# Kernel tuning notes

Hardware: AMD Instinct MI355X
Metric: run time of the kernel (lower is better)

## Reference

```python
import jax, jax.numpy as jnp
import numpy as np

N_QUBITS = 10
T_STEPS = 10
NDATA = 1024
DIM = 2 ** N_QUBITS
PI = float(np.pi)


def setup_inputs() -> dict:
    key = jax.random.key(0)
    k1, k2, k3, k4, k5 = jax.random.split(key, 5)
    # random complex amplitudes (normalized to unit states inside reference)
    inputs_re = jax.random.normal(k1, (NDATA, DIM), dtype=jnp.float32)
    inputs_im = jax.random.normal(k2, (NDATA, DIM), dtype=jnp.float32)
    # diffusion noise schedule diff_hs (t,) in (0,1]
    diff_hs = jax.random.uniform(k5, (T_STEPS,), dtype=jnp.float32, minval=0.1, maxval=1.0)
    # var_1 = diff_hs.repeat(3n) in torch == tile -> index k scaled by diff_hs[k % t]
    var_1 = jnp.tile(diff_hs, 3 * N_QUBITS)                                  # (3*n*t,)
    phis = (jax.random.uniform(k3, (NDATA, 3 * N_QUBITS * T_STEPS), dtype=jnp.float32)
            * (PI / 4.0) - (PI / 8.0)) * var_1[None, :]
    gs = (jax.random.uniform(k4, (NDATA, T_STEPS), dtype=jnp.float32) * 0.2 + 0.4) * diff_hs[None, :]
    return {"inputs_re": inputs_re, "inputs_im": inputs_im, "phis": phis, "gs": gs}


def _apply_1q(psi, M, i):
    """Apply per-sample 2x2 gate M (B,2,2) on qubit i (qubit 0 = MSB) to psi (B, 2**n)."""
    left = 2 ** i
    right = 2 ** (N_QUBITS - 1 - i)
    s = psi.reshape(NDATA, left, 2, right)
    s = jnp.einsum('bxy,bayc->baxc', M, s)
    return s.reshape(NDATA, DIM)


def _scramble(inputs_re, inputs_im, phis, gs):
    n, t = N_QUBITS, T_STEPS
    psi = (inputs_re + 1j * inputs_im).astype(jnp.complex64)
    psi = psi / jnp.linalg.norm(psi, axis=1, keepdims=True)  # unit input states

    # precompute sum_{i<j} z_i z_j per basis state for the diagonal RZZ product
    idx = jnp.arange(DIM)
    bits = (idx[:, None] >> jnp.arange(n - 1, -1, -1)[None, :]) & 1  # (DIM, n), qubit0=MSB
    z = 1.0 - 2.0 * bits.astype(jnp.float32)
    zsum = z.sum(axis=1)
    pairsum = 0.5 * (zsum ** 2 - n)                                   # (DIM,)
    inv = 1.0 / (2.0 * np.sqrt(float(n)))

    for tt in range(t):
        base = 3 * n * tt
        for i in range(n):
            a = phis[:, base + i]            # first RZ angle
            th = phis[:, base + n + i]       # RY angle
            b = phis[:, base + 2 * n + i]    # second RZ angle
            c = jnp.cos(0.5 * th).astype(jnp.complex64)
            s = jnp.sin(0.5 * th).astype(jnp.complex64)
            ea_m = jnp.exp(-0.5j * a); ea_p = jnp.exp(0.5j * a)
            eb_m = jnp.exp(-0.5j * b); eb_p = jnp.exp(0.5j * b)
            # M = RZ(b) @ RY(th) @ RZ(a), per sample (B,2,2)
            M = jnp.stack([
                jnp.stack([eb_m * c * ea_m, -eb_m * s * ea_p], axis=-1),
                jnp.stack([eb_p * s * ea_m,  eb_p * c * ea_p], axis=-1),
            ], axis=-2)
            psi = _apply_1q(psi, M, i)
        # all RZZ(i,j, theta) gates are diagonal with shared theta -> single fused phase
        theta = (gs[:, tt] * inv).astype(jnp.complex64)
        psi = psi * jnp.exp(-0.5j * theta[:, None] * pairsum[None, :])
    return psi


def reference(inputs_re, inputs_im, phis, gs):
    psi = _scramble(inputs_re, inputs_im, phis, gs)
    return jnp.stack([psi.real, psi.imag])  # (2, Ndata, 2**n) float32
```

## Files before the change

### kernel.cpp

```cpp
#include <hip/hip_runtime.h>

#define NQ 10
#define TS 10
#define DIM 1024
#define ND 1024

typedef _Float16 h4 __attribute__((ext_vector_type(4)));
typedef __fp16  p2 __attribute__((ext_vector_type(2)));
typedef float f4 __attribute__((ext_vector_type(4)));

__device__ __forceinline__ f4 mfma16(h4 a, h4 b, f4 c) {
    return __builtin_amdgcn_mfma_f32_16x16x16f16(a, b, c, 0, 0, 0);
}
__device__ __forceinline__ h4 cvt_h4(f4 x) {
    p2 lo = __builtin_amdgcn_cvt_pkrtz(x[0], x[1]);
    p2 hi = __builtin_amdgcn_cvt_pkrtz(x[2], x[3]);
    h4 r; r[0] = lo[0]; r[1] = lo[1]; r[2] = hi[0]; r[3] = hi[1];
    return r;
}
__device__ __forceinline__ float hsel(int ob, int ib, float cq, float sq) {
    return (ob == ib) ? cq : (ob ? sq : -sq);
}

__global__ __launch_bounds__(64, 1) void qsim_kernel(
    const float* __restrict__ re_in, const float* __restrict__ im_in,
    const float* __restrict__ phis, const float* __restrict__ gs,
    float* __restrict__ out)
{
    const int sample = blockIdx.x;
    const int lane = threadIdx.x;
    const int quad = lane >> 4;
    const int cc = lane & 15;
    const int c3 = (cc >> 3) & 1, c2 = (cc >> 2) & 1, c1 = (cc >> 1) & 1, c0 = cc & 1;
    const int q1 = quad >> 1, q0 = quad & 1;

    const float* pr_in = re_in + sample * DIM;
    const float* pi_in = im_in + sample * DIM;
    const float* ph = phis + sample * (3 * NQ * TS);
    const float* gsp = gs + sample * TS;

    f4 Sr[4], Si[4];
    const int lbase = 256 * quad + cc;
#pragma unroll
    for (int n = 0; n < 4; ++n)
#pragma unroll
        for (int s = 0; s < 4; ++s) {
            Sr[n][s] = pr_in[lbase + 64 * s + 16 * n];
            Si[n][s] = pi_in[lbase + 64 * s + 16 * n];
        }

    const float inv = 0.15811388300841897f;
    float gk[TS];
#pragma unroll
    for (int t = 0; t < TS; ++t) gk[t] = -0.5f * (gsp[t] * inv);

    float nrm = 0.f;
#pragma unroll
    for (int n = 0; n < 4; ++n)
#pragma unroll
        for (int s = 0; s < 4; ++s) nrm += Sr[n][s] * Sr[n][s] + Si[n][s] * Si[n][s];
#pragma unroll
    for (int off = 32; off >= 1; off >>= 1) nrm += __shfl_xor(nrm, off, 64);
    const float scl = rsqrtf(nrm);
#pragma unroll
    for (int n = 0; n < 4; ++n) { Sr[n] *= scl; Si[n] *= scl; }

    float psv[4][4];
    const int pbase = __popc(quad) + __popc(cc);
#pragma unroll
    for (int n = 0; n < 4; ++n)
#pragma unroll
        for (int s = 0; s < 4; ++s) {
            const int p = pbase + __popc(n) + __popc(s);
            const int z = NQ - 2 * p;
            psv[n][s] = 0.5f * (float)(z * z - NQ);
        }
    const float fq1 = (float)q1, fq0 = (float)q0;
    const float fc3 = (float)c3, fc2 = (float)c2, fc1 = (float)c1, fc0 = (float)c0;

    float DCP[4][4], DSP[4][4];
    h4 gb; h4 hb[4][4];
    float bcur[NQ];

    auto make_trig = [&](const float* v, float kcur, float dcp[4][4], float dsp[4][4]) {
        float sv = 0.f;
#pragma unroll
        for (int i = 0; i < NQ; ++i) sv += v[i];
        float base = fmaf(-0.5f, sv, 0.f);
        base = fmaf(fq1, v[0], base); base = fmaf(fq0, v[1], base);
        base = fmaf(fc3, v[6], base); base = fmaf(fc2, v[7], base);
        base = fmaf(fc1, v[8], base); base = fmaf(fc0, v[9], base);
        const float addS[4] = {0.f, v[3], v[2], v[2] + v[3]};
        const float addN[4] = {0.f, v[5], v[4], v[4] + v[5]};
#pragma unroll
        for (int n = 0; n < 4; ++n)
#pragma unroll
            for (int s = 0; s < 4; ++s) {
                const float phi = fmaf(kcur, psv[n][s], base + addN[n] + addS[s]);
                float sp, cp;
                __sincosf(phi, &sp, &cp);
                dcp[n][s] = cp;
                dsp[n][s] = sp;
            }
    };
    auto make_tiles = [&](const float* th_src, h4& gbo, h4 hbo[4][4]) {
        float C[NQ], S[NQ];
#pragma unroll
        for (int g = 0; g < NQ; ++g) {
            float sg, cg;
            __sincosf(0.5f * th_src[g], &sg, &cg);
            S[g] = sg; C[g] = cg;
        }
        {
            const float f01 = hsel(c3, q1, C[0], S[0]) * hsel(c2, q0, C[1], S[1]);
            float e[4];
#pragma unroll
            for (int s = 0; s < 4; ++s)
                e[s] = f01 * hsel(c1, s >> 1, C[2], S[2]) * hsel(c0, s & 1, C[3], S[3]);
            p2 lo = __builtin_amdgcn_cvt_pkrtz(e[0], e[1]);
            p2 hi = __builtin_amdgcn_cvt_pkrtz(e[2], e[3]);
            gbo[0] = lo[0]; gbo[1] = lo[1]; gbo[2] = hi[0]; gbo[3] = hi[1];
        }
        const float F67 = hsel(c3, q1, C[6], S[6]) * hsel(c2, q0, C[7], S[7]);
        float F89[4];
#pragma unroll
        for (int s = 0; s < 4; ++s)
            F89[s] = F67 * hsel(c1, s >> 1, C[8], S[8]) * hsel(c0, s & 1, C[9], S[9]);
#pragma unroll
        for (int n = 0; n < 4; ++n)
#pragma unroll
            for (int j = 0; j < 4; ++j) {
                const float F45 = hsel(n >> 1, j >> 1, C[4], S[4])
                                * hsel(n & 1,  j & 1,  C[5], S[5]);
                p2 lo = __builtin_amdgcn_cvt_pkrtz(F45 * F89[0], F45 * F89[1]);
                p2 hi = __builtin_amdgcn_cvt_pkrtz(F45 * F89[2], F45 * F89[3]);
                hbo[n][j][0] = lo[0]; hbo[n][j][1] = lo[1];
                hbo[n][j][2] = hi[0]; hbo[n][j][3] = hi[1];
            }
    };

    {
        float phs0[30];
#pragma unroll
        for (int j = 0; j < 30; ++j) phs0[j] = ph[j];
        make_trig(&phs0[0], 0.f, DCP, DSP);
        make_tiles(&phs0[10], gb, hb);
#pragma unroll
        for (int i = 0; i < NQ; ++i) bcur[i] = phs0[20 + i];
    }
    float pipe[2][30];
#pragma unroll
    for (int j = 0; j < 30; ++j) pipe[0][j] = ph[30 + j];

    const f4 zf4 = {0.f, 0.f, 0.f, 0.f};

#pragma unroll
    for (int tt = 0; tt < TS; ++tt) {
#pragma unroll
        for (int n = 0; n < 4; ++n)
#pragma unroll
            for (int s = 0; s < 4; ++s) {
                const float cp = DCP[n][s], sp = DSP[n][s];
                const float xr = Sr[n][s], xi = Si[n][s];
                Sr[n][s] = cp * xr - sp * xi;
                Si[n][s] = sp * xr + cp * xi;
            }

        if (tt + 2 < TS) {
#pragma unroll
            for (int j = 0; j < 30; ++j) pipe[(tt + 1) & 1][j] = ph[30 * (tt + 2) + j];
        }

        h4 ar[4], ai[4];
#pragma unroll
        for (int n = 0; n < 4; ++n) { ar[n] = cvt_h4(Sr[n]); ai[n] = cvt_h4(Si[n]); }
        f4 Tr[4], Ti[4];
#pragma unroll
        for (int n = 0; n < 4; ++n) {
            Tr[n] = mfma16(ar[n], gb, zf4);
            Ti[n] = mfma16(ai[n], gb, zf4);
        }
        h4 tr[4], ti[4];
#pragma unroll
        for (int n = 0; n < 4; ++n) { tr[n] = cvt_h4(Tr[n]); ti[n] = cvt_h4(Ti[n]); }
#pragma unroll
        for (int n = 0; n < 4; ++n) {
            f4 accr = zf4, acci = zf4;
#pragma unroll
            for (int j = 0; j < 4; ++j) {
                accr = mfma16(tr[j], hb[n][j], accr);
                acci = mfma16(ti[j], hb[n][j], acci);
            }
            Sr[n] = accr;
            Si[n] = acci;
        }

        if (tt + 1 < TS) {
            const float* pN = pipe[tt & 1];
            float vN[NQ];
#pragma unroll
            for (int i = 0; i < NQ; ++i) vN[i] = pN[i] + bcur[i];
            make_trig(vN, gk[tt], DCP, DSP);
            make_tiles(&pN[10], gb, hb);
#pragma unroll
            for (int i = 0; i < NQ; ++i) bcur[i] = pN[20 + i];
        } else {
            make_trig(bcur, gk[TS - 1], DCP, DSP);
        }
    }

#pragma unroll
    for (int n = 0; n < 4; ++n)
#pragma unroll
        for (int s = 0; s < 4; ++s) {
            const float cp = DCP[n][s], sp = DSP[n][s];
            const float xr = Sr[n][s], xi = Si[n][s];
            Sr[n][s] = cp * xr - sp * xi;
            Si[n][s] = sp * xr + cp * xi;
        }

    float* outr = out + sample * DIM;
    float* outi = out + ND * DIM + sample * DIM;
#pragma unroll
    for (int n = 0; n < 4; ++n)
#pragma unroll
        for (int s = 0; s < 4; ++s) {
            outr[lbase + 64 * s + 16 * n] = Sr[n][s];
            outi[lbase + 64 * s + 16 * n] = Si[n][s];
        }
}

extern "C" void kernel_launch(void* const* d_in, const int* in_sizes, int n_in,
                              void* d_out, int out_size, void* d_ws, size_t ws_size,
                              hipStream_t stream) {
    const float* re_in = (const float*)d_in[0];
    const float* im_in = (const float*)d_in[1];
    const float* phis  = (const float*)d_in[2];
    const float* gs    = (const float*)d_in[3];
    float* out = (float*)d_out;
    qsim_kernel<<<ND, 64, 0, stream>>>(re_in, im_in, phis, gs, out);
}
```

Before: 77.83 us.

## Double-buffer gate tiles and interleave next-step trig with MFMA chains

Gate tile registers become double-buffered so the next step's trig and tile construction can be placed between the first and second MFMA stages. This hides transcendental and ALU latency behind matrix work. The second-stage accumulation is split into two independent chains that are summed afterward, which shortens the MFMA dependency chain. The sign-select helper is replaced by sign-bit XOR and shared product tables, which cuts per-step ALU work at the cost of more register pressure from the duplicated tiles.

Result: no change. 77.47 us (-0.5%).

```diff
diff --git a/kernel.cpp b/kernel.cpp
--- a/kernel.cpp
+++ b/kernel.cpp
@@ -18,8 +18,8 @@
     h4 r; r[0] = lo[0]; r[1] = lo[1]; r[2] = hi[0]; r[3] = hi[1];
     return r;
 }
-__device__ __forceinline__ float hsel(int ob, int ib, float cq, float sq) {
-    return (ob == ib) ? cq : (ob ? sq : -sq);
+__device__ __forceinline__ float xsgn(float v, unsigned m) {
+    return __uint_as_float(__float_as_uint(v) ^ m);
 }
 
 __global__ __launch_bounds__(64, 1) void qsim_kernel(
@@ -34,6 +34,13 @@
     const int c3 = (cc >> 3) & 1, c2 = (cc >> 2) & 1, c1 = (cc >> 1) & 1, c0 = cc & 1;
     const int q1 = quad >> 1, q0 = quad & 1;
 
+    const bool e31 = (c3 == q1);
+    const bool e20 = (c2 == q0);
+    const bool bc1 = (c1 != 0);
+    const bool bc0 = (c0 != 0);
+    const unsigned sg3 = c3 ? 0u : 0x80000000u;
+    const unsigned sg2 = c2 ? 0u : 0x80000000u;
+
     const float* pr_in = re_in + sample * DIM;
     const float* pi_in = im_in + sample * DIM;
     const float* ph = phis + sample * (3 * NQ * TS);
@@ -78,15 +85,16 @@
     const float fq1 = (float)q1, fq0 = (float)q0;
     const float fc3 = (float)c3, fc2 = (float)c2, fc1 = (float)c1, fc0 = (float)c0;
 
-    float DCP[4][4], DSP[4][4];
-    h4 gb; h4 hb[4][4];
+    f4 DCPv[4], DSPv[4];
+    h4 gbb[2];
+    h4 hbb[2][4][4];
     float bcur[NQ];
 
-    auto make_trig = [&](const float* v, float kcur, float dcp[4][4], float dsp[4][4]) {
+    auto make_trig = [&](const float* v, float kcur) {
         float sv = 0.f;
 #pragma unroll
         for (int i = 0; i < NQ; ++i) sv += v[i];
-        float base = fmaf(-0.5f, sv, 0.f);
+        float base = -0.5f * sv;
         base = fmaf(fq1, v[0], base); base = fmaf(fq0, v[1], base);
         base = fmaf(fc3, v[6], base); base = fmaf(fc2, v[7], base);
         base = fmaf(fc1, v[8], base); base = fmaf(fc0, v[9], base);
@@ -99,41 +107,55 @@
                 const float phi = fmaf(kcur, psv[n][s], base + addN[n] + addS[s]);
                 float sp, cp;
                 __sincosf(phi, &sp, &cp);
-                dcp[n][s] = cp;
-                dsp[n][s] = sp;
+                DCPv[n][s] = cp;
+                DSPv[n][s] = sp;
             }
     };
-    auto make_tiles = [&](const float* th_src, h4& gbo, h4 hbo[4][4]) {
+
+    auto make_tiles = [&](const float* th, h4& gbo, h4 (&hbo)[4][4]) {
         float C[NQ], S[NQ];
 #pragma unroll
         for (int g = 0; g < NQ; ++g) {
             float sg, cg;
-            __sincosf(0.5f * th_src[g], &sg, &cg);
+            __sincosf(0.5f * th[g], &sg, &cg);
             S[g] = sg; C[g] = cg;
         }
         {
-            const float f01 = hsel(c3, q1, C[0], S[0]) * hsel(c2, q0, C[1], S[1]);
-            float e[4];
-#pragma unroll
-            for (int s = 0; s < 4; ++s)
-                e[s] = f01 * hsel(c1, s >> 1, C[2], S[2]) * hsel(c0, s & 1, C[3], S[3]);
-            p2 lo = __builtin_amdgcn_cvt_pkrtz(e[0], e[1]);
-            p2 hi = __builtin_amdgcn_cvt_pkrtz(e[2], e[3]);
+            const float g0 = e31 ? C[0] : xsgn(S[0], sg3);
+            const float g1 = e20 ? C[1] : xsgn(S[1], sg2);
+            const float f01 = g0 * g1;
+            const float A0 = bc1 ? S[2] : C[2];
+            const float A1 = bc1 ? C[2] : -S[2];
+            const float B0 = bc0 ? S[3] : C[3];
+            const float B1 = bc0 ? C[3] : -S[3];
+            p2 lo = __builtin_amdgcn_cvt_pkrtz(f01 * A0 * B0, f01 * A0 * B1);
+            p2 hi = __builtin_amdgcn_cvt_pkrtz(f01 * A1 * B0, f01 * A1 * B1);
             gbo[0] = lo[0]; gbo[1] = lo[1]; gbo[2] = hi[0]; gbo[3] = hi[1];
         }
-        const float F67 = hsel(c3, q1, C[6], S[6]) * hsel(c2, q0, C[7], S[7]);
-        float F89[4];
-#pragma unroll
-        for (int s = 0; s < 4; ++s)
-            F89[s] = F67 * hsel(c1, s >> 1, C[8], S[8]) * hsel(c0, s & 1, C[9], S[9]);
+        const float F67 = (e31 ? C[6] : xsgn(S[6], sg3)) * (e20 ? C[7] : xsgn(S[7], sg2));
+        const float A0p = bc1 ? S[8] : C[8];
+        const float A1p = bc1 ? C[8] : -S[8];
+        const float B0p = bc0 ? S[9] : C[9];
+        const float B1p = bc0 ? C[9] : -S[9];
+        float W[4];
+        W[0] = F67 * A0p * B0p; W[1] = F67 * A0p * B1p;
+        W[2] = F67 * A1p * B0p; W[3] = F67 * A1p * B1p;
+        const float P4[4] = {C[4] * C[5], C[4] * S[5], S[4] * C[5], S[4] * S[5]};
+        float TP[4][4];
+#pragma unroll
+        for (int k = 0; k < 4; ++k)
+#pragma unroll
+            for (int s = 0; s < 4; ++s) TP[k][s] = P4[k] * W[s];
 #pragma unroll
         for (int n = 0; n < 4; ++n)
 #pragma unroll
             for (int j = 0; j < 4; ++j) {
-                const float F45 = hsel(n >> 1, j >> 1, C[4], S[4])
-                                * hsel(n & 1,  j & 1,  C[5], S[5]);
-                p2 lo = __builtin_amdgcn_cvt_pkrtz(F45 * F89[0], F45 * F89[1]);
-                p2 hi = __builtin_amdgcn_cvt_pkrtz(F45 * F89[2], F45 * F89[3]);
+                const int n1 = n >> 1, n0 = n & 1, j1 = j >> 1, j0 = j & 1;
+                const int d1 = n1 ^ j1, d0 = n0 ^ j0;
+                const int idx = d1 * 2 + d0;
+                const float sg = (((d1 && !n1) ? -1.f : 1.f) * ((d0 && !n0) ? -1.f : 1.f));
+                p2 lo = __builtin_amdgcn_cvt_pkrtz(sg * TP[idx][0], sg * TP[idx][1]);
+                p2 hi = __builtin_amdgcn_cvt_pkrtz(sg * TP[idx][2], sg * TP[idx][3]);
                 hbo[n][j][0] = lo[0]; hbo[n][j][1] = lo[1];
                 hbo[n][j][2] = hi[0]; hbo[n][j][3] = hi[1];
             }
@@ -143,8 +165,8 @@
         float phs0[30];
 #pragma unroll
         for (int j = 0; j < 30; ++j) phs0[j] = ph[j];
-        make_trig(&phs0[0], 0.f, DCP, DSP);
-        make_tiles(&phs0[10], gb, hb);
+        make_trig(&phs0[0], 0.f);
+        make_tiles(&phs0[10], gbb[0], hbb[0]);
 #pragma unroll
         for (int i = 0; i < NQ; ++i) bcur[i] = phs0[20 + i];
     }
@@ -157,14 +179,11 @@
 #pragma unroll
     for (int tt = 0; tt < TS; ++tt) {
 #pragma unroll
-        for (int n = 0; n < 4; ++n)
-#pragma unroll
-            for (int s = 0; s < 4; ++s) {
-                const float cp = DCP[n][s], sp = DSP[n][s];
-                const float xr = Sr[n][s], xi = Si[n][s];
-                Sr[n][s] = cp * xr - sp * xi;
-                Si[n][s] = sp * xr + cp * xi;
-            }
+        for (int n = 0; n < 4; ++n) {
+            const f4 xr = Sr[n], xi = Si[n];
+            Sr[n] = DCPv[n] * xr - DSPv[n] * xi;
+            Si[n] = DSPv[n] * xr + DCPv[n] * xi;
+        }
 
         if (tt + 2 < TS) {
 #pragma unroll
@@ -177,22 +196,8 @@
         f4 Tr[4], Ti[4];
 #pragma unroll
         for (int n = 0; n < 4; ++n) {
-            Tr[n] = mfma16(ar[n], gb, zf4);
-            Ti[n] = mfma16(ai[n], gb, zf4);
-        }
-        h4 tr[4], ti[4];
-#pragma unroll
-        for (int n = 0; n < 4; ++n) { tr[n] = cvt_h4(Tr[n]); ti[n] = cvt_h4(Ti[n]); }
-#pragma unroll
-        for (int n = 0; n < 4; ++n) {
-            f4 accr = zf4, acci = zf4;
-#pragma unroll
-            for (int j = 0; j < 4; ++j) {
-                accr = mfma16(tr[j], hb[n][j], accr);
-                acci = mfma16(ti[j], hb[n][j], acci);
-            }
-            Sr[n] = accr;
-            Si[n] = acci;
+            Tr[n] = mfma16(ar[n], gbb[tt & 1], zf4);
+            Ti[n] = mfma16(ai[n], gbb[tt & 1], zf4);
         }
 
         if (tt + 1 < TS) {
@@ -200,24 +205,38 @@
             float vN[NQ];
 #pragma unroll
             for (int i = 0; i < NQ; ++i) vN[i] = pN[i] + bcur[i];
-            make_trig(vN, gk[tt], DCP, DSP);
-            make_tiles(&pN[10], gb, hb);
+            make_trig(vN, gk[tt]);
+            make_tiles(&pN[10], gbb[(tt + 1) & 1], hbb[(tt + 1) & 1]);
 #pragma unroll
             for (int i = 0; i < NQ; ++i) bcur[i] = pN[20 + i];
         } else {
-            make_trig(bcur, gk[TS - 1], DCP, DSP);
+            make_trig(bcur, gk[TS - 1]);
+        }
+
+        h4 tr[4], ti[4];
+#pragma unroll
+        for (int n = 0; n < 4; ++n) { tr[n] = cvt_h4(Tr[n]); ti[n] = cvt_h4(Ti[n]); }
+#pragma unroll
+        for (int n = 0; n < 4; ++n) {
+            f4 r0 = mfma16(tr[0], hbb[tt & 1][n][0], zf4);
+            r0 = mfma16(tr[1], hbb[tt & 1][n][1], r0);
+            f4 r1 = mfma16(tr[2], hbb[tt & 1][n][2], zf4);
+            r1 = mfma16(tr[3], hbb[tt & 1][n][3], r1);
+            f4 i0 = mfma16(ti[0], hbb[tt & 1][n][0], zf4);
+            i0 = mfma16(ti[1], hbb[tt & 1][n][1], i0);
+            f4 i1 = mfma16(ti[2], hbb[tt & 1][n][2], zf4);
+            i1 = mfma16(ti[3], hbb[tt & 1][n][3], i1);
+            Sr[n] = r0 + r1;
+            Si[n] = i0 + i1;
         }
     }
 
 #pragma unroll
-    for (int n = 0; n < 4; ++n)
-#pragma unroll
-        for (int s = 0; s < 4; ++s) {
-            const float cp = DCP[n][s], sp = DSP[n][s];
-            const float xr = Sr[n][s], xi = Si[n][s];
-            Sr[n][s] = cp * xr - sp * xi;
-            Si[n][s] = sp * xr + cp * xi;
-        }
+    for (int n = 0; n < 4; ++n) {
+        const f4 xr = Sr[n], xi = Si[n];
+        Sr[n] = DCPv[n] * xr - DSPv[n] * xi;
+        Si[n] = DSPv[n] * xr + DCPv[n] * xi;
+    }
 
     float* outr = out + sample * DIM;
     float* outi = out + ND * DIM + sample * DIM;
```
